# Kernel optimization log

Measured on AMD Instinct MI355X. Metric: run time of the kernel, lower is better.

The kernel has to match this reference:

```python
import jax, jax.numpy as jnp
import numpy as np

EPS = 1e-5
TEMP = 0.2  # contrastive temperature


def setup_inputs() -> dict:
    key = jax.random.key(0)
    ks_ = jax.random.split(key, 16)
    N, d, d_free, D, F_ = 10000, 32, 32, 64, 3
    x = jax.random.normal(ks_[0], (N, 256), dtype=jnp.float32)
    feats = jax.random.normal(ks_[1], (F_, N, d), dtype=jnp.float32)
    feat_free = 0.01 * jax.random.normal(ks_[2], (N, d_free), dtype=jnp.float32)
    # curvatures: k = init_curvature * randn(); keep away from 0 so the curved branch is taken
    ks = jax.random.uniform(ks_[3], (F_,), dtype=jnp.float32) + 0.5
    Ws = jax.random.normal(ks_[4], (F_, D, d), dtype=jnp.float32)
    Ws = Ws / jnp.linalg.norm(Ws, axis=-1, keepdims=True)  # row-normalized as in __init__
    bias = 2.0 * jnp.pi * jax.random.uniform(ks_[5], (F_, D), dtype=jnp.float32)
    W_free = jax.random.normal(ks_[6], (D, d_free), dtype=jnp.float32)
    W_free = W_free / jnp.linalg.norm(W_free, axis=-1, keepdims=True)
    b_free = 2.0 * jnp.pi * jax.random.uniform(ks_[7], (D,), dtype=jnp.float32)
    W1 = 0.05 * jax.random.normal(ks_[8], (3 * d, 64), dtype=jnp.float32)
    b1 = jnp.zeros((64,), dtype=jnp.float32)
    W2 = 0.05 * jax.random.normal(ks_[9], (64, 1), dtype=jnp.float32)
    b2 = jnp.zeros((1,), dtype=jnp.float32)
    motif = jax.random.randint(ks_[10], (3, 50000), 0, N, dtype=jnp.int32)
    neg_uv = jax.random.randint(ks_[11], (2, 50000), 0, N, dtype=jnp.int32)
    return {"x": x, "feats": feats, "feat_free": feat_free, "ks": ks,
            "Ws": Ws, "bias": bias, "W_free": W_free, "b_free": b_free,
            "W1": W1, "b1": b1, "W2": W2, "b2": b2,
            "motif": motif, "neg_uv": neg_uv}


def _normalize(xf, k):
    # RiemannianFeatures.normalize with the random scale fixed at 0.5 for determinism
    radius = 1.0 / jnp.sqrt(jnp.abs(k))
    xn = jnp.linalg.norm(xf, axis=-1, keepdims=True)
    return xf / xn * (0.9 * 0.5) * radius


def _mlp(f3, W1, b1, W2, b2):
    return jax.nn.relu(f3 @ W1 + b1) @ W2 + b2  # [M, 1]


def _gather3(feat, m):
    # nodes_from_motif: concat features of u, v, w
    return jnp.concatenate([feat[m[0]], feat[m[1]], feat[m[2]]], axis=-1)


def reference(x, feats, feat_free, ks, Ws, bias, W_free, b_free,
              W1, b1, W2, b2, motif, neg_uv):
    F_, N, d = feats.shape
    d_free = feat_free.shape[-1]

    # ---- RiemannianFeatures.forward: normalized products per factor + free part
    products = [_normalize(feats[i], ks[i]) for i in range(F_)]
    products.append(feat_free)

    # ---- random_mapping: pairwise manifold distance -> exp/cos transform
    zs = []
    for i in range(F_):
        xi, w, b, k = products[i], Ws[i], bias[i], ks[i]
        div = jnp.sum((xi[:, None, :] - w[None, :, :]) ** 2, axis=-1)      # [N, D]
        num = 1.0 + k * jnp.sum(xi * xi, axis=-1, keepdims=True)           # [N, 1]
        dist = jnp.log(num / (div + EPS))
        zs.append(jnp.exp((d - 1) * dist * 0.5) * jnp.cos(dist + b))
    dist_f = feat_free @ W_free.T                                          # Euclidean branch
    zs.append(jnp.exp((d_free - 1) * dist_f * 0.5) * jnp.cos(dist_f + b_free))
    x2 = jnp.concatenate(zs, axis=-1)                                      # [N, embed]

    # ---- cal_cl_loss: full N x N cosine-similarity contrastive loss
    n1 = jnp.linalg.norm(x, axis=-1)
    n2 = jnp.linalg.norm(x2, axis=-1)
    sim = jnp.einsum('ik,jk->ij', x, x2) / (n1[:, None] * n2[None, :])
    sim = jnp.exp(sim / TEMP)
    pos = jnp.diagonal(sim)
    loss_1 = -jnp.mean(jnp.log(pos / (jnp.sum(sim, axis=0) - pos)))
    loss_2 = -jnp.mean(jnp.log(pos / (jnp.sum(sim, axis=1) - pos)))
    cl_loss = 0.5 * (loss_1 + loss_2)

    # ---- cal_motif_loss: gather triples -> MLP -> BCE (neg via provided sampled pairs)
    neg_motif = jnp.concatenate([neg_uv, motif[2:3]], axis=0)
    motif_loss = jnp.float32(0.0)
    for p in products:
        pos_logit = _mlp(_gather3(p, motif), W1, b1, W2, b2)
        neg_logit = _mlp(_gather3(p, neg_motif), W1, b1, W2, b2)
        motif_loss = motif_loss \
            - jnp.mean(jax.nn.log_sigmoid(pos_logit)) \
            - jnp.mean(jax.nn.log_sigmoid(-neg_logit))

    return cl_loss + motif_loss
```

## Files before the change

kernel.cpp:

```cpp
#include <hip/hip_runtime.h>
#include <hip/hip_bf16.h>
#include <math.h>

#define EMBED 256
#define NF 3
#define DD 64
#define BM 128
#define BN 128
#define BKF 128
#define MOTIF_BLOCKS 2048

typedef unsigned short ushort_t;
typedef unsigned char uchar_t;
typedef float f32x4 __attribute__((ext_vector_type(4)));
typedef float f32x2 __attribute__((ext_vector_type(2)));

__device__ __forceinline__ void gl2lds16(const void* g, void* l) {
    __builtin_amdgcn_global_load_lds(
        (const __attribute__((address_space(1))) unsigned int*)g,
        (__attribute__((address_space(3))) unsigned int*)l, 16, 0, 0);
}

__device__ __forceinline__ uchar_t f2fp8(float f) {
    int p = __builtin_amdgcn_cvt_pk_fp8_f32(f, f, 0, false);
    return (uchar_t)(p & 0xff);
}
template<bool HI>
__device__ __forceinline__ f32x2 pk2(unsigned int w) {
    return __builtin_amdgcn_cvt_pk_f32_fp8((int)w, HI);
}

__global__ __launch_bounds__(256) void k_embed(
    const float* __restrict__ x,
    const float* __restrict__ feats,
    const float* __restrict__ feat_free,
    const float* __restrict__ ks,
    const float* __restrict__ Ws,
    const float* __restrict__ bias,
    const float* __restrict__ W_free,
    const float* __restrict__ b_free,
    float* __restrict__ p_out,
    uchar_t* __restrict__ xnf8,
    uchar_t* __restrict__ x2nf8,
    float* __restrict__ zero_base,
    int N, int Npad)
{
    int wave = threadIdx.x >> 6;
    int t    = threadIdx.x & 63;
    int n = blockIdx.x * 4 + wave;
    int gid = blockIdx.x * 256 + threadIdx.x;
    if (gid < 2*N) zero_base[gid] = 0.f;

    __shared__ float Wl[128*65];
    __shared__ float xi_s[4][NF][32];
    __shared__ float ff_s[4][32];

    for (int e = threadIdx.x; e < NF*DD*32; e += 256) {
        int i = e >> 11, rem = e & 2047, tr = rem >> 5, c = rem & 31;
        Wl[(i*32 + c)*65 + tr] = Ws[e];
    }
    for (int e = threadIdx.x; e < DD*32; e += 256) {
        int tr = e >> 5, c = e & 31;
        Wl[(96 + c)*65 + tr] = W_free[e];
    }

    bool active = (n < N);
    if (!active && n < Npad) {
        ((int*)(xnf8  + (size_t)n*EMBED))[t] = 0;
        ((int*)(x2nf8 + (size_t)n*EMBED))[t] = 0;
    }

    float (*xi)[32] = xi_s[wave];
    float* ffs = ff_s[wave];

    float v[NF];
    float ffv = 0.f;
    if (active && t < 32) {
        #pragma unroll
        for (int i = 0; i < NF; ++i) v[i] = feats[((size_t)i*N + n)*32 + t];
        ffv = feat_free[(size_t)n*32 + t];
    } else {
        #pragma unroll
        for (int i = 0; i < NF; ++i) v[i] = 0.f;
    }

    float num[NF];
    #pragma unroll
    for (int i = 0; i < NF; ++i) {
        float s = v[i]*v[i];
        s += __shfl_xor(s, 1, 64);  s += __shfl_xor(s, 2, 64);
        s += __shfl_xor(s, 4, 64);  s += __shfl_xor(s, 8, 64);
        s += __shfl_xor(s, 16, 64);
        s = __shfl(s, 0, 64);
        float k = ks[i];
        float scale = 0.45f / (sqrtf(s) * sqrtf(fabsf(k)));
        float xv = v[i] * scale;
        if (active && t < 32) {
            xi[i][t] = xv;
            p_out[((size_t)i*N + n)*32 + t] = xv;
        }
        num[i] = 1.0f + k * (scale*scale*s);
    }
    if (active && t < 32) ffs[t] = ffv;
    __syncthreads();
    if (!active) return;

    float z[4];
    float zsq = 0.f;
    #pragma unroll
    for (int i = 0; i < NF; ++i) {
        float div = 0.f;
        #pragma unroll
        for (int c = 0; c < 32; ++c) {
            float d = xi[i][c] - Wl[(i*32 + c)*65 + t];
            div += d*d;
        }
        float dist = __logf(num[i] / (div + 1e-5f));
        float zz = __expf(15.5f * dist) * __cosf(dist + bias[i*DD + t]);
        z[i] = zz;
        zsq += zz*zz;
    }
    {
        float dot = 0.f;
        #pragma unroll
        for (int c = 0; c < 32; ++c) dot = fmaf(ffs[c], Wl[(96 + c)*65 + t], dot);
        float zz = __expf(15.5f * dot) * __cosf(dot + b_free[t]);
        z[3] = zz;
        zsq += zz*zz;
    }
    zsq += __shfl_xor(zsq, 1, 64);  zsq += __shfl_xor(zsq, 2, 64);
    zsq += __shfl_xor(zsq, 4, 64);  zsq += __shfl_xor(zsq, 8, 64);
    zsq += __shfl_xor(zsq, 16, 64); zsq += __shfl_xor(zsq, 32, 64);
    float iv2 = 1.0f / sqrtf(zsq);

    #pragma unroll
    for (int i = 0; i < NF; ++i) x2nf8[(size_t)n*EMBED + i*DD + t] = f2fp8(z[i]*iv2);
    x2nf8[(size_t)n*EMBED + 192 + t] = f2fp8(z[3]*iv2);

    float xv[4];
    float s1 = 0.f;
    #pragma unroll
    for (int q = 0; q < 4; ++q) { xv[q] = x[(size_t)n*EMBED + q*64 + t]; s1 += xv[q]*xv[q]; }
    s1 += __shfl_xor(s1, 1, 64);  s1 += __shfl_xor(s1, 2, 64);
    s1 += __shfl_xor(s1, 4, 64);  s1 += __shfl_xor(s1, 8, 64);
    s1 += __shfl_xor(s1, 16, 64); s1 += __shfl_xor(s1, 32, 64);
    float iv1 = 5.0f / sqrtf(s1);
    #pragma unroll
    for (int q = 0; q < 4; ++q) xnf8[(size_t)n*EMBED + q*64 + t] = f2fp8(xv[q]*iv1);
}

__global__ __launch_bounds__(256) void k_mlp1(
    const float* __restrict__ p,
    const float* __restrict__ feat_free,
    const float* __restrict__ W1,
    const float* __restrict__ b1,
    uchar_t* __restrict__ H,
    int N)
{
    int lane = threadIdx.x & 63;
    int gw = (blockIdx.x * blockDim.x + threadIdx.x) >> 6;
    int nwaves = (gridDim.x * blockDim.x) >> 6;

    float wcol[96];
    #pragma unroll
    for (int c = 0; c < 96; ++c) wcol[c] = W1[c*64 + lane];
    float b1l = b1[lane];

    int total = 4 * N;
    for (int unit = gw; unit < total; unit += nwaves) {
        int node = __builtin_amdgcn_readfirstlane(unit >> 2);
        int prod = __builtin_amdgcn_readfirstlane(unit & 3);
        const float* P = (prod < 3) ? (p + ((size_t)prod*N + node)*32)
                                    : (feat_free + (size_t)node*32);
        float fc[32];
        #pragma unroll
        for (int c = 0; c < 32; ++c) fc[c] = P[c];
        #pragma unroll
        for (int s = 0; s < 3; ++s) {
            float h = (s == 2) ? b1l : 0.f;
            #pragma unroll
            for (int c = 0; c < 32; ++c) h = fmaf(fc[c], wcol[s*32 + c], h);
            H[(((size_t)prod*3 + s)*N + node)*64 + lane] = f2fp8(h);
        }
    }
}

__global__ __launch_bounds__(256) void k_motif3(
    const uchar_t* __restrict__ H,
    const int* __restrict__ motif,
    const int* __restrict__ neg_uv,
    const float* __restrict__ W2,
    const float* __restrict__ b2,
    float* __restrict__ partials,
    int N, int M)
{
    int lane = threadIdx.x & 63;
    int sub  = lane >> 3;
    int ch   = (lane & 7) * 8;
    int caseId = blockIdx.x & 7;
    int rank   = (blockIdx.x >> 3) * 4 + (threadIdx.x >> 6);
    int prod  = caseId >> 1;
    int isneg = caseId & 1;
    const uchar_t* Hu = H + ((size_t)prod*3 + 0)*N*64;
    const uchar_t* Hv = H + ((size_t)prod*3 + 1)*N*64;
    const uchar_t* Hw = H + ((size_t)prod*3 + 2)*N*64;
    const int* iu = isneg ? neg_uv       : motif;
    const int* iv = isneg ? (neg_uv + M) : (motif + M);
    const int* iw = motif + 2*M;

    float w2c[8];
    #pragma unroll
    for (int c = 0; c < 8; ++c) w2c[c] = W2[ch + c];
    float b2v = b2[0];

    float accl = 0.f;
    #pragma unroll 2
    for (int r0 = rank*8; r0 < M; r0 += 8192) {
        int r = r0 + sub;
        bool ok = (r < M);
        int rc = ok ? r : 0;
        int u = iu[rc], v = iv[rc], w = iw[rc];
        uint2 du = *(const uint2*)&Hu[(size_t)u*64 + ch];
        uint2 dv = *(const uint2*)&Hv[(size_t)v*64 + ch];
        uint2 dw = *(const uint2*)&Hw[(size_t)w*64 + ch];
        float pl = 0.f;
        {
            f32x2 s;
            s = pk2<false>(du.x) + pk2<false>(dv.x) + pk2<false>(dw.x);
            pl = fmaf(fmaxf(s.x,0.f), w2c[0], pl);  pl = fmaf(fmaxf(s.y,0.f), w2c[1], pl);
            s = pk2<true>(du.x) + pk2<true>(dv.x) + pk2<true>(dw.x);
            pl = fmaf(fmaxf(s.x,0.f), w2c[2], pl);  pl = fmaf(fmaxf(s.y,0.f), w2c[3], pl);
            s = pk2<false>(du.y) + pk2<false>(dv.y) + pk2<false>(dw.y);
            pl = fmaf(fmaxf(s.x,0.f), w2c[4], pl);  pl = fmaf(fmaxf(s.y,0.f), w2c[5], pl);
            s = pk2<true>(du.y) + pk2<true>(dv.y) + pk2<true>(dw.y);
            pl = fmaf(fmaxf(s.x,0.f), w2c[6], pl);  pl = fmaf(fmaxf(s.y,0.f), w2c[7], pl);
        }
        pl += __shfl_xor(pl, 1, 64);
        pl += __shfl_xor(pl, 2, 64);
        pl += __shfl_xor(pl, 4, 64);
        float logit = pl + b2v;
        float z = isneg ? -logit : logit;
        float sp = fmaxf(-z, 0.f) + __logf(1.f + __expf(-fabsf(z)));
        accl -= ok ? sp : 0.f;
    }
    #pragma unroll
    for (int m = 1; m < 64; m <<= 1) accl += __shfl_xor(accl, m, 64);

    __shared__ float wred[4];
    if (lane == 0) wred[threadIdx.x >> 6] = accl;
    __syncthreads();
    if (threadIdx.x == 0)
        partials[blockIdx.x] = (wred[0] + wred[1] + wred[2] + wred[3]) * 0.125f;
}

__global__ __launch_bounds__(256) void k_sim(
    const uchar_t* __restrict__ xn, const uchar_t* __restrict__ x2n,
    float* __restrict__ rowsum, float* __restrict__ colsum, float* __restrict__ pos,
    int N, int nb)
{
    __shared__ __align__(16) uchar_t As[BM*BKF];
    __shared__ __align__(16) uchar_t Bs[BN*BKF];
    __shared__ float rsum_s[BM];
    __shared__ float csum_s[BN];

    int tid  = threadIdx.x;
    int lane = tid & 63;
    int w    = tid >> 6;
    int wr   = w >> 1, wc = w & 1;
    int quad = lane >> 4, l15 = lane & 15;

    int pid = blockIdx.x;
    int per_group = 8 * nb;
    int group = pid / per_group;
    int rem = pid - group * per_group;
    int rowspan = min(8, nb - group * 8);
    int prow = group * 8 + rem % rowspan;
    int pcol = rem / rowspan;
    int row0 = prow * BM, col0 = pcol * BN;

    if (tid < BM) { rsum_s[tid] = 0.f; csum_s[tid] = 0.f; }

    f32x4 acc[4][4];
    #pragma unroll
    for (int i = 0; i < 4; ++i)
        #pragma unroll
        for (int j = 0; j < 4; ++j) acc[i][j] = (f32x4){0.f,0.f,0.f,0.f};

    for (int kt = 0; kt < EMBED; kt += BKF) {
        #pragma unroll
        for (int i = 0; i < 4; ++i) {
            int slot = i*256 + tid;
            int r = slot >> 3, c = slot & 7;
            int sc = c ^ (r & 7);
            gl2lds16(xn  + (size_t)(row0 + r)*EMBED + kt + sc*16, &As[slot*16]);
            gl2lds16(x2n + (size_t)(col0 + r)*EMBED + kt + sc*16, &Bs[slot*16]);
        }
        __syncthreads();
        #pragma unroll
        for (int s = 0; s < 4; ++s) {
            long a[4], b[4];
            int g = s*2 + (quad >> 1);
            int sub8 = (quad & 1) * 8;
            #pragma unroll
            for (int ti = 0; ti < 4; ++ti) {
                int ra = wr*64 + ti*16 + l15;
                a[ti] = *(const long*)&As[ra*BKF + (g ^ (ra & 7))*16 + sub8];
            }
            #pragma unroll
            for (int tj = 0; tj < 4; ++tj) {
                int rb = wc*64 + tj*16 + l15;
                b[tj] = *(const long*)&Bs[rb*BKF + (g ^ (rb & 7))*16 + sub8];
            }
            #pragma unroll
            for (int ti = 0; ti < 4; ++ti)
                #pragma unroll
                for (int tj = 0; tj < 4; ++tj)
                    acc[ti][tj] = __builtin_amdgcn_mfma_f32_16x16x32_fp8_fp8(a[ti], b[tj], acc[ti][tj], 0, 0, 0);
        }
        __syncthreads();
    }

    #pragma unroll
    for (int ti = 0; ti < 4; ++ti) {
        #pragma unroll
        for (int tj = 0; tj < 4; ++tj) {
            #pragma unroll
            for (int r = 0; r < 4; ++r) {
                int gi = row0 + wr*64 + ti*16 + quad*4 + r;
                int gj = col0 + wc*64 + tj*16 + l15;
                float e = 0.f;
                if (gi < N && gj < N) {
                    e = __expf(acc[ti][tj][r]);
                    if (gi == gj) pos[gi] = e;
                }
                acc[ti][tj][r] = e;
            }
        }
    }
    #pragma unroll
    for (int ti = 0; ti < 4; ++ti) {
        #pragma unroll
        for (int r = 0; r < 4; ++r) {
            float rsv = acc[ti][0][r] + acc[ti][1][r] + acc[ti][2][r] + acc[ti][3][r];
            rsv += __shfl_xor(rsv, 1, 64);
            rsv += __shfl_xor(rsv, 2, 64);
            rsv += __shfl_xor(rsv, 4, 64);
            rsv += __shfl_xor(rsv, 8, 64);
            if (l15 == 0) atomicAdd(&rsum_s[wr*64 + ti*16 + quad*4 + r], rsv);
        }
    }
    #pragma unroll
    for (int tj = 0; tj < 4; ++tj) {
        float csv = 0.f;
        #pragma unroll
        for (int ti = 0; ti < 4; ++ti)
            #pragma unroll
            for (int r = 0; r < 4; ++r) csv += acc[ti][tj][r];
        csv += __shfl_xor(csv, 16, 64);
        csv += __shfl_xor(csv, 32, 64);
        if (lane < 16) atomicAdd(&csum_s[wc*64 + tj*16 + lane], csv);
    }
    __syncthreads();
    if (tid < BM) {
        int gi = row0 + tid;
        if (gi < N) atomicAdd(&rowsum[gi], rsum_s[tid]);
        int gj = col0 + tid;
        if (gj < N) atomicAdd(&colsum[gj], csum_s[tid]);
    }
}

__global__ __launch_bounds__(256) void k_final(
    const float* __restrict__ rowsum, const float* __restrict__ colsum,
    const float* __restrict__ pos, const float* __restrict__ partials,
    float* __restrict__ out, int N, int M, int nparts)
{
    __shared__ float red1[256], red2[256], red3[256];
    int t = threadIdx.x;
    float l1 = 0.f, l2 = 0.f, mo = 0.f;
    for (int i = t; i < N; i += 256) {
        float pv = pos[i];
        l1 += __logf((colsum[i] - pv) / pv);
        l2 += __logf((rowsum[i] - pv) / pv);
    }
    for (int i = t; i < nparts; i += 256) mo += partials[i];
    red1[t] = l1; red2[t] = l2; red3[t] = mo; __syncthreads();
    for (int s = 128; s > 0; s >>= 1) {
        if (t < s) { red1[t] += red1[t+s]; red2[t] += red2[t+s]; red3[t] += red3[t+s]; }
        __syncthreads();
    }
    if (t == 0) {
        float cl = 0.5f * (red1[0] + red2[0]) / (float)N;
        out[0] = cl - red3[0] / (float)M;
    }
}

extern "C" void kernel_launch(void* const* d_in, const int* in_sizes, int n_in,
                              void* d_out, int out_size, void* d_ws, size_t ws_size,
                              hipStream_t stream)
{
    const float* x         = (const float*)d_in[0];
    const float* feats     = (const float*)d_in[1];
    const float* feat_free = (const float*)d_in[2];
    const float* ks        = (const float*)d_in[3];
    const float* Ws        = (const float*)d_in[4];
    const float* bias      = (const float*)d_in[5];
    const float* W_free    = (const float*)d_in[6];
    const float* b_free    = (const float*)d_in[7];
    const float* W1        = (const float*)d_in[8];
    const float* b1        = (const float*)d_in[9];
    const float* W2        = (const float*)d_in[10];
    const float* b2        = (const float*)d_in[11];
    const int*   motif     = (const int*)d_in[12];
    const int*   neg_uv    = (const int*)d_in[13];
    int N = in_sizes[0] / EMBED;
    int M = in_sizes[13] / 2;
    int nb = (N + BM - 1) / BM;
    int Npad = nb * BM;

    uchar_t* xnf8  = (uchar_t*)d_ws;
    uchar_t* x2nf8 = xnf8 + (size_t)Npad*EMBED;
    uchar_t* H8    = x2nf8 + (size_t)Npad*EMBED;
    float* p      = (float*)(H8 + (size_t)12*N*64);
    float* posv   = p + (size_t)3*N*32;
    float* rowsum = posv + N;
    float* colsum = rowsum + N;
    float* partials = colsum + N;

    k_embed<<<(Npad + 3) / 4, 256, 0, stream>>>(x, feats, feat_free, ks, Ws, bias,
                                                W_free, b_free, p, xnf8, x2nf8,
                                                rowsum, N, Npad);
    k_mlp1<<<512, 256, 0, stream>>>(p, feat_free, W1, b1, H8, N);
    k_motif3<<<MOTIF_BLOCKS, 256, 0, stream>>>(H8, motif, neg_uv, W2, b2, partials, N, M);
    k_sim<<<nb * nb, 256, 0, stream>>>(xnf8, x2nf8, rowsum, colsum, posv, N, nb);
    k_final<<<1, 256, 0, stream>>>(rowsum, colsum, posv, partials, (float*)d_out, N, M, MOTIF_BLOCKS);
}
```

Before: 257.8 us.

## Widen similarity tiles to 256x128 and make embed kernel grid-stride persistent

The similarity kernel now uses 256x128 tiles, and each wave owns 64 rows across all 128 columns. Each B fragment read from LDS therefore feeds four MFMAs, and the rows no longer need shared atomics. This roughly halves the block count and the global rowsum/colsum atomics, at the cost of doubling the accumulator registers per wave. The embed kernel becomes a fixed 256-block grid-stride loop, so the weight-matrix LDS staging is paid once per block rather than once per four nodes. Padding rows are zeroed separately for the now-different A and B padded sizes.

```diff
diff --git a/kernel.cpp b/kernel.cpp
--- a/kernel.cpp
+++ b/kernel.cpp
@@ -5,8 +5,8 @@
 #define EMBED 256
 #define NF 3
 #define DD 64
-#define BM 128
-#define BN 128
+#define BM2 256
+#define BN2 128
 #define BKF 128
 #define MOTIF_BLOCKS 2048
 
@@ -43,110 +43,119 @@
     uchar_t* __restrict__ xnf8,
     uchar_t* __restrict__ x2nf8,
     float* __restrict__ zero_base,
-    int N, int Npad)
-{
-    int wave = threadIdx.x >> 6;
-    int t    = threadIdx.x & 63;
-    int n = blockIdx.x * 4 + wave;
-    int gid = blockIdx.x * 256 + threadIdx.x;
-    if (gid < 2*N) zero_base[gid] = 0.f;
+    int N, int NpadM, int NpadN)
+{
+    int tid  = threadIdx.x;
+    int wave = tid >> 6;
+    int t    = tid & 63;
+    int gtid = blockIdx.x * 256 + tid;
+    int stride = gridDim.x * 256;
+
+    for (int i = gtid; i < 2*N; i += stride) zero_base[i] = 0.f;
+    {
+        int padA = (NpadM - N) * (EMBED/4);
+        int* pa = (int*)(xnf8 + (size_t)N*EMBED);
+        for (int i = gtid; i < padA; i += stride) pa[i] = 0;
+        int padB = (NpadN - N) * (EMBED/4);
+        int* pb = (int*)(x2nf8 + (size_t)N*EMBED);
+        for (int i = gtid; i < padB; i += stride) pb[i] = 0;
+    }
 
     __shared__ float Wl[128*65];
     __shared__ float xi_s[4][NF][32];
     __shared__ float ff_s[4][32];
 
-    for (int e = threadIdx.x; e < NF*DD*32; e += 256) {
+    for (int e = tid; e < NF*DD*32; e += 256) {
         int i = e >> 11, rem = e & 2047, tr = rem >> 5, c = rem & 31;
         Wl[(i*32 + c)*65 + tr] = Ws[e];
     }
-    for (int e = threadIdx.x; e < DD*32; e += 256) {
+    for (int e = tid; e < DD*32; e += 256) {
         int tr = e >> 5, c = e & 31;
         Wl[(96 + c)*65 + tr] = W_free[e];
     }
-
-    bool active = (n < N);
-    if (!active && n < Npad) {
-        ((int*)(xnf8  + (size_t)n*EMBED))[t] = 0;
-        ((int*)(x2nf8 + (size_t)n*EMBED))[t] = 0;
-    }
+    __syncthreads();
 
     float (*xi)[32] = xi_s[wave];
     float* ffs = ff_s[wave];
-
-    float v[NF];
-    float ffv = 0.f;
-    if (active && t < 32) {
-        #pragma unroll
-        for (int i = 0; i < NF; ++i) v[i] = feats[((size_t)i*N + n)*32 + t];
-        ffv = feat_free[(size_t)n*32 + t];
-    } else {
-        #pragma unroll
-        for (int i = 0; i < NF; ++i) v[i] = 0.f;
-    }
-
-    float num[NF];
-    #pragma unroll
-    for (int i = 0; i < NF; ++i) {
-        float s = v[i]*v[i];
-        s += __shfl_xor(s, 1, 64);  s += __shfl_xor(s, 2, 64);
-        s += __shfl_xor(s, 4, 64);  s += __shfl_xor(s, 8, 64);
-        s += __shfl_xor(s, 16, 64);
-        s = __shfl(s, 0, 64);
-        float k = ks[i];
-        float scale = 0.45f / (sqrtf(s) * sqrtf(fabsf(k)));
-        float xv = v[i] * scale;
-        if (active && t < 32) {
-            xi[i][t] = xv;
-            p_out[((size_t)i*N + n)*32 + t] = xv;
-        }
-        num[i] = 1.0f + k * (scale*scale*s);
-    }
-    if (active && t < 32) ffs[t] = ffv;
-    __syncthreads();
-    if (!active) return;
-
-    float z[4];
-    float zsq = 0.f;
-    #pragma unroll
-    for (int i = 0; i < NF; ++i) {
-        float div = 0.f;
-        #pragma unroll
-        for (int c = 0; c < 32; ++c) {
-            float d = xi[i][c] - Wl[(i*32 + c)*65 + t];
-            div += d*d;
-        }
-        float dist = __logf(num[i] / (div + 1e-5f));
-        float zz = __expf(15.5f * dist) * __cosf(dist + bias[i*DD + t]);
-        z[i] = zz;
-        zsq += zz*zz;
-    }
-    {
-        float dot = 0.f;
-        #pragma unroll
-        for (int c = 0; c < 32; ++c) dot = fmaf(ffs[c], Wl[(96 + c)*65 + t], dot);
-        float zz = __expf(15.5f * dot) * __cosf(dot + b_free[t]);
-        z[3] = zz;
-        zsq += zz*zz;
-    }
-    zsq += __shfl_xor(zsq, 1, 64);  zsq += __shfl_xor(zsq, 2, 64);
-    zsq += __shfl_xor(zsq, 4, 64);  zsq += __shfl_xor(zsq, 8, 64);
-    zsq += __shfl_xor(zsq, 16, 64); zsq += __shfl_xor(zsq, 32, 64);
-    float iv2 = 1.0f / sqrtf(zsq);
-
-    #pragma unroll
-    for (int i = 0; i < NF; ++i) x2nf8[(size_t)n*EMBED + i*DD + t] = f2fp8(z[i]*iv2);
-    x2nf8[(size_t)n*EMBED + 192 + t] = f2fp8(z[3]*iv2);
-
-    float xv[4];
-    float s1 = 0.f;
-    #pragma unroll
-    for (int q = 0; q < 4; ++q) { xv[q] = x[(size_t)n*EMBED + q*64 + t]; s1 += xv[q]*xv[q]; }
-    s1 += __shfl_xor(s1, 1, 64);  s1 += __shfl_xor(s1, 2, 64);
-    s1 += __shfl_xor(s1, 4, 64);  s1 += __shfl_xor(s1, 8, 64);
-    s1 += __shfl_xor(s1, 16, 64); s1 += __shfl_xor(s1, 32, 64);
-    float iv1 = 5.0f / sqrtf(s1);
-    #pragma unroll
-    for (int q = 0; q < 4; ++q) xnf8[(size_t)n*EMBED + q*64 + t] = f2fp8(xv[q]*iv1);
+    int ngroups = (N + 3) >> 2;
+
+    for (int grp = blockIdx.x; grp < ngroups; grp += gridDim.x) {
+        int n = grp*4 + wave;
+        if (n >= N) continue;
+
+        float v[NF];
+        float ffv = 0.f;
+        if (t < 32) {
+            #pragma unroll
+            for (int i = 0; i < NF; ++i) v[i] = feats[((size_t)i*N + n)*32 + t];
+            ffv = feat_free[(size_t)n*32 + t];
+        } else {
+            #pragma unroll
+            for (int i = 0; i < NF; ++i) v[i] = 0.f;
+        }
+
+        float num[NF];
+        #pragma unroll
+        for (int i = 0; i < NF; ++i) {
+            float s = v[i]*v[i];
+            s += __shfl_xor(s, 1, 64);  s += __shfl_xor(s, 2, 64);
+            s += __shfl_xor(s, 4, 64);  s += __shfl_xor(s, 8, 64);
+            s += __shfl_xor(s, 16, 64);
+            s = __shfl(s, 0, 64);
+            float k = ks[i];
+            float scale = 0.45f / (sqrtf(s) * sqrtf(fabsf(k)));
+            float xv = v[i] * scale;
+            if (t < 32) {
+                xi[i][t] = xv;
+                p_out[((size_t)i*N + n)*32 + t] = xv;
+            }
+            num[i] = 1.0f + k * (scale*scale*s);
+        }
+        if (t < 32) ffs[t] = ffv;
+
+        float z[4];
+        float zsq = 0.f;
+        #pragma unroll
+        for (int i = 0; i < NF; ++i) {
+            float div = 0.f;
+            #pragma unroll
+            for (int c = 0; c < 32; ++c) {
+                float d = xi[i][c] - Wl[(i*32 + c)*65 + t];
+                div += d*d;
+            }
+            float dist = __logf(num[i] / (div + 1e-5f));
+            float zz = __expf(15.5f * dist) * __cosf(dist + bias[i*DD + t]);
+            z[i] = zz;
+            zsq += zz*zz;
+        }
+        {
+            float dot = 0.f;
+            #pragma unroll
+            for (int c = 0; c < 32; ++c) dot = fmaf(ffs[c], Wl[(96 + c)*65 + t], dot);
+            float zz = __expf(15.5f * dot) * __cosf(dot + b_free[t]);
+            z[3] = zz;
+            zsq += zz*zz;
+        }
+        zsq += __shfl_xor(zsq, 1, 64);  zsq += __shfl_xor(zsq, 2, 64);
+        zsq += __shfl_xor(zsq, 4, 64);  zsq += __shfl_xor(zsq, 8, 64);
+        zsq += __shfl_xor(zsq, 16, 64); zsq += __shfl_xor(zsq, 32, 64);
+        float iv2 = 1.0f / sqrtf(zsq);
+
+        #pragma unroll
+        for (int i = 0; i < NF; ++i) x2nf8[(size_t)n*EMBED + i*DD + t] = f2fp8(z[i]*iv2);
+        x2nf8[(size_t)n*EMBED + 192 + t] = f2fp8(z[3]*iv2);
+
+        float xv[4];
+        float s1 = 0.f;
+        #pragma unroll
+        for (int q = 0; q < 4; ++q) { xv[q] = x[(size_t)n*EMBED + q*64 + t]; s1 += xv[q]*xv[q]; }
+        s1 += __shfl_xor(s1, 1, 64);  s1 += __shfl_xor(s1, 2, 64);
+        s1 += __shfl_xor(s1, 4, 64);  s1 += __shfl_xor(s1, 8, 64);
+        s1 += __shfl_xor(s1, 16, 64); s1 += __shfl_xor(s1, 32, 64);
+        float iv1 = 5.0f / sqrtf(s1);
+        #pragma unroll
+        for (int q = 0; q < 4; ++q) xnf8[(size_t)n*EMBED + q*64 + t] = f2fp8(xv[q]*iv1);
+    }
 }
 
 __global__ __launch_bounds__(256) void k_mlp1(
@@ -256,66 +265,69 @@
 __global__ __launch_bounds__(256) void k_sim(
     const uchar_t* __restrict__ xn, const uchar_t* __restrict__ x2n,
     float* __restrict__ rowsum, float* __restrict__ colsum, float* __restrict__ pos,
-    int N, int nb)
-{
-    __shared__ __align__(16) uchar_t As[BM*BKF];
-    __shared__ __align__(16) uchar_t Bs[BN*BKF];
-    __shared__ float rsum_s[BM];
-    __shared__ float csum_s[BN];
+    int N, int nbm, int nbn)
+{
+    __shared__ __align__(16) uchar_t As[BM2*BKF];
+    __shared__ __align__(16) uchar_t Bs[BN2*BKF];
+    __shared__ float rsum_s[BM2];
+    __shared__ float csum_s[BN2];
 
     int tid  = threadIdx.x;
     int lane = tid & 63;
     int w    = tid >> 6;
-    int wr   = w >> 1, wc = w & 1;
     int quad = lane >> 4, l15 = lane & 15;
 
     int pid = blockIdx.x;
-    int per_group = 8 * nb;
+    int per_group = 8 * nbn;
     int group = pid / per_group;
     int rem = pid - group * per_group;
-    int rowspan = min(8, nb - group * 8);
+    int rowspan = min(8, nbm - group * 8);
     int prow = group * 8 + rem % rowspan;
     int pcol = rem / rowspan;
-    int row0 = prow * BM, col0 = pcol * BN;
-
-    if (tid < BM) { rsum_s[tid] = 0.f; csum_s[tid] = 0.f; }
-
-    f32x4 acc[4][4];
+    int row0 = prow * BM2, col0 = pcol * BN2;
+
+    if (tid < BN2) csum_s[tid] = 0.f;
+
+    f32x4 acc[4][8];
     #pragma unroll
     for (int i = 0; i < 4; ++i)
         #pragma unroll
-        for (int j = 0; j < 4; ++j) acc[i][j] = (f32x4){0.f,0.f,0.f,0.f};
+        for (int j = 0; j < 8; ++j) acc[i][j] = (f32x4){0.f,0.f,0.f,0.f};
 
     for (int kt = 0; kt < EMBED; kt += BKF) {
+        #pragma unroll
+        for (int i = 0; i < 8; ++i) {
+            int slot = i*256 + tid;
+            int r = slot >> 3, c = slot & 7;
+            int sc = c ^ (r & 7);
+            gl2lds16(xn + (size_t)(row0 + r)*EMBED + kt + sc*16, &As[slot*16]);
+        }
         #pragma unroll
         for (int i = 0; i < 4; ++i) {
             int slot = i*256 + tid;
             int r = slot >> 3, c = slot & 7;
             int sc = c ^ (r & 7);
-            gl2lds16(xn  + (size_t)(row0 + r)*EMBED + kt + sc*16, &As[slot*16]);
             gl2lds16(x2n + (size_t)(col0 + r)*EMBED + kt + sc*16, &Bs[slot*16]);
         }
         __syncthreads();
         #pragma unroll
         for (int s = 0; s < 4; ++s) {
-            long a[4], b[4];
             int g = s*2 + (quad >> 1);
             int sub8 = (quad & 1) * 8;
+            long a[4];
             #pragma unroll
             for (int ti = 0; ti < 4; ++ti) {
-                int ra = wr*64 + ti*16 + l15;
+                int ra = w*64 + ti*16 + l15;
                 a[ti] = *(const long*)&As[ra*BKF + (g ^ (ra & 7))*16 + sub8];
             }
             #pragma unroll
-            for (int tj = 0; tj < 4; ++tj) {
-                int rb = wc*64 + tj*16 + l15;
-                b[tj] = *(const long*)&Bs[rb*BKF + (g ^ (rb & 7))*16 + sub8];
+            for (int tj = 0; tj < 8; ++tj) {
+                int rb = tj*16 + l15;
+                long b = *(const long*)&Bs[rb*BKF + (g ^ (rb & 7))*16 + sub8];
+                #pragma unroll
+                for (int ti = 0; ti < 4; ++ti)
+                    acc[ti][tj] = __builtin_amdgcn_mfma_f32_16x16x32_fp8_fp8(a[ti], b, acc[ti][tj], 0, 0, 0);
             }
-            #pragma unroll
-            for (int ti = 0; ti < 4; ++ti)
-                #pragma unroll
-                for (int tj = 0; tj < 4; ++tj)
-                    acc[ti][tj] = __builtin_amdgcn_mfma_f32_16x16x32_fp8_fp8(a[ti], b[tj], acc[ti][tj], 0, 0, 0);
         }
         __syncthreads();
     }
@@ -323,11 +335,11 @@
     #pragma unroll
     for (int ti = 0; ti < 4; ++ti) {
         #pragma unroll
-        for (int tj = 0; tj < 4; ++tj) {
+        for (int tj = 0; tj < 8; ++tj) {
             #pragma unroll
             for (int r = 0; r < 4; ++r) {
-                int gi = row0 + wr*64 + ti*16 + quad*4 + r;
-                int gj = col0 + wc*64 + tj*16 + l15;
+                int gi = row0 + w*64 + ti*16 + quad*4 + r;
+                int gj = col0 + tj*16 + l15;
                 float e = 0.f;
                 if (gi < N && gj < N) {
                     e = __expf(acc[ti][tj][r]);
@@ -341,16 +353,18 @@
     for (int ti = 0; ti < 4; ++ti) {
         #pragma unroll
         for (int r = 0; r < 4; ++r) {
-            float rsv = acc[ti][0][r] + acc[ti][1][r] + acc[ti][2][r] + acc[ti][3][r];
+            float rsv = 0.f;
+            #pragma unroll
+            for (int tj = 0; tj < 8; ++tj) rsv += acc[ti][tj][r];
             rsv += __shfl_xor(rsv, 1, 64);
             rsv += __shfl_xor(rsv, 2, 64);
             rsv += __shfl_xor(rsv, 4, 64);
             rsv += __shfl_xor(rsv, 8, 64);
-            if (l15 == 0) atomicAdd(&rsum_s[wr*64 + ti*16 + quad*4 + r], rsv);
-        }
-    }
-    #pragma unroll
-    for (int tj = 0; tj < 4; ++tj) {
+            if (l15 == 0) rsum_s[w*64 + ti*16 + quad*4 + r] = rsv;
+        }
+    }
+    #pragma unroll
+    for (int tj = 0; tj < 8; ++tj) {
         float csv = 0.f;
         #pragma unroll
         for (int ti = 0; ti < 4; ++ti)
@@ -358,14 +372,16 @@
             for (int r = 0; r < 4; ++r) csv += acc[ti][tj][r];
         csv += __shfl_xor(csv, 16, 64);
         csv += __shfl_xor(csv, 32, 64);
-        if (lane < 16) atomicAdd(&csum_s[wc*64 + tj*16 + lane], csv);
+        if (lane < 16) atomicAdd(&csum_s[tj*16 + lane], csv);
     }
     __syncthreads();
-    if (tid < BM) {
+    {
         int gi = row0 + tid;
         if (gi < N) atomicAdd(&rowsum[gi], rsum_s[tid]);
-        int gj = col0 + tid;
-        if (gj < N) atomicAdd(&colsum[gj], csum_s[tid]);
+        if (tid < BN2) {
+            int gj = col0 + tid;
+            if (gj < N) atomicAdd(&colsum[gj], csum_s[tid]);
+        }
     }
 }
 
@@ -414,23 +430,25 @@
     const int*   neg_uv    = (const int*)d_in[13];
     int N = in_sizes[0] / EMBED;
     int M = in_sizes[13] / 2;
-    int nb = (N + BM - 1) / BM;
-    int Npad = nb * BM;
+    int nbm = (N + BM2 - 1) / BM2;
+    int nbn = (N + BN2 - 1) / BN2;
+    int NpadM = nbm * BM2;
+    int NpadN = nbn * BN2;
 
     uchar_t* xnf8  = (uchar_t*)d_ws;
-    uchar_t* x2nf8 = xnf8 + (size_t)Npad*EMBED;
-    uchar_t* H8    = x2nf8 + (size_t)Npad*EMBED;
+    uchar_t* x2nf8 = xnf8 + (size_t)NpadM*EMBED;
+    uchar_t* H8    = x2nf8 + (size_t)NpadN*EMBED;
     float* p      = (float*)(H8 + (size_t)12*N*64);
     float* posv   = p + (size_t)3*N*32;
     float* rowsum = posv + N;
     float* colsum = rowsum + N;
     float* partials = colsum + N;
 
-    k_embed<<<(Npad + 3) / 4, 256, 0, stream>>>(x, feats, feat_free, ks, Ws, bias,
-                                                W_free, b_free, p, xnf8, x2nf8,
-                                                rowsum, N, Npad);
+    k_embed<<<256, 256, 0, stream>>>(x, feats, feat_free, ks, Ws, bias,
+                                     W_free, b_free, p, xnf8, x2nf8,
+                                     rowsum, N, NpadM, NpadN);
     k_mlp1<<<512, 256, 0, stream>>>(p, feat_free, W1, b1, H8, N);
     k_motif3<<<MOTIF_BLOCKS, 256, 0, stream>>>(H8, motif, neg_uv, W2, b2, partials, N, M);
-    k_sim<<<nb * nb, 256, 0, stream>>>(xnf8, x2nf8, rowsum, colsum, posv, N, nb);
+    k_sim<<<nbm * nbn, 256, 0, stream>>>(xnf8, x2nf8, rowsum, colsum, posv, N, nbm, nbn);
     k_final<<<1, 256, 0, stream>>>(rowsum, colsum, posv, partials, (float*)d_out, N, M, MOTIF_BLOCKS);
 }
```

Result: slower. 314.4 us (+22.0%).
